# Performance work log

Measured on AMD Instinct MI355X. Metric: run time of the kernel, lower is better.

The kernel has to match this reference:

```python
import jax, jax.numpy as jnp
import numpy as np

NUM_CONN = 8

def _ein_reduce(f):
    # Einstein t-norm fold over last axis: T(a,b) = ab / (2 - (a+b-ab))
    acc = f[..., 0]
    for i in range(1, f.shape[-1]):
        b = f[..., i]
        ab = acc * b
        acc = ab / (2.0 - (acc + b - ab))
    return acc

def _coein_reduce(f):
    # Einstein t-conorm fold over last axis: S(a,b) = (a+b) / (1 + ab)
    acc = f[..., 0]
    for i in range(1, f.shape[-1]):
        b = f[..., i]
        acc = (acc + b) / (1.0 + acc * b)
    return acc

def _ddlg_layer(x, w, idx, is_train):
    # x: [B, in], idx: [out, C] int, w: [out, 4]
    feats = x[:, idx]                      # [B, out, C] gather
    ops = jnp.stack([
        jnp.min(feats, axis=-1),
        jnp.max(feats, axis=-1),
        _ein_reduce(feats),
        _coein_reduce(feats),
    ], axis=-1)                            # [B, out, 4]
    if is_train:
        prob = jax.nn.softmax(w, axis=-1)  # [out, 4]
    else:
        prob = jax.nn.one_hot(jnp.argmax(w, axis=-1), 4, dtype=x.dtype)
    return jnp.einsum('bof,of->bo', ops, prob)

def setup_inputs() -> dict:
    key = jax.random.key(0)
    ks = jax.random.split(key, 6)
    sizes = [4096, 2048, 1024, 2048, 4096]
    x = jax.random.uniform(ks[0], (4096, sizes[0]), dtype=jnp.float32)
    ws = [jax.random.normal(ks[1 + i], (sizes[i + 1], 4), dtype=jnp.float32) for i in range(4)]
    rng = np.random.default_rng(0)
    idxs = []
    for i in range(4):
        # randperm-without-replacement per output neuron
        perm = np.argsort(rng.random((sizes[i + 1], sizes[i])), axis=-1)[:, :NUM_CONN]
        idxs.append(jnp.asarray(perm, dtype=jnp.int32))
    return {
        'x': x,
        'w0': ws[0], 'w1': ws[1], 'w2': ws[2], 'w3': ws[3],
        'idx0': idxs[0], 'idx1': idxs[1], 'idx2': idxs[2], 'idx3': idxs[3],
        'is_train': 1,
    }

def reference(x, w0, w1, w2, w3, idx0, idx1, idx2, idx3, is_train):
    h = _ddlg_layer(x, w0, idx0, is_train)
    h = _ddlg_layer(h, w1, idx1, is_train)
    h = _ddlg_layer(h, w2, idx2, is_train)
    h = _ddlg_layer(h, w3, idx3, is_train)
    return h
```

## Files before the change

### kernel.cpp

```cpp
#include <hip/hip_runtime.h>


typedef _Float16 h2 __attribute__((ext_vector_type(2)));
typedef _Float16 h4 __attribute__((ext_vector_type(4)));

__device__ __forceinline__ float fastrcp(float x) { return __builtin_amdgcn_rcpf(x); }
__device__ __forceinline__ _Float16 hrcp(_Float16 x) {
#if __has_builtin(__builtin_amdgcn_rcph)
    return __builtin_amdgcn_rcph(x);
#else
    return (_Float16)__builtin_amdgcn_rcpf((float)x);
#endif
}
__device__ __forceinline__ h2 splat2(_Float16 s) { h2 v = {s, s}; return v; }
__device__ __forceinline__ unsigned packh2(float a, float b) {
    h2 v = {(_Float16)a, (_Float16)b};
    return __builtin_bit_cast(unsigned, v);
}

__global__ __launch_bounds__(256) void prep_k(const float* __restrict__ w0,
                                              const float* __restrict__ w1,
                                              const float* __restrict__ w2,
                                              const float* __restrict__ w3,
                                              const int* __restrict__ is_train,
                                              h4* __restrict__ probsH) {
    const int g = blockIdx.x * 256 + threadIdx.x;
    const float* w; int o;
    if (g < 2048)      { w = w0; o = g; }
    else if (g < 3072) { w = w1; o = g - 2048; }
    else if (g < 5120) { w = w2; o = g - 3072; }
    else               { w = w3; o = g - 5120; }
    float wv[4];
#pragma unroll
    for (int c = 0; c < 4; ++c) wv[c] = w[(o << 2) + c];
    float p[4];
    if (*is_train) {
        float m = fmaxf(fmaxf(wv[0], wv[1]), fmaxf(wv[2], wv[3]));
        float s = 0.0f;
#pragma unroll
        for (int c = 0; c < 4; ++c) { p[c] = __expf(wv[c] - m); s += p[c]; }
        float inv = fastrcp(s);
#pragma unroll
        for (int c = 0; c < 4; ++c) p[c] *= inv;
    } else {
        int a = 0; float best = wv[0];
#pragma unroll
        for (int c = 1; c < 4; ++c) if (wv[c] > best) { best = wv[c]; a = c; }
#pragma unroll
        for (int c = 0; c < 4; ++c) p[c] = (c == a) ? 1.0f : 0.0f;
    }
    probsH[g] = h4{(_Float16)p[0], (_Float16)p[1], (_Float16)p[2], (_Float16)p[3]};
}

struct Chain { h2 mn, mx, De, Ne, Nc, Dc; };

__device__ __forceinline__ h2 row_at(const unsigned* __restrict__ rows, int i) {
    return __builtin_bit_cast(h2, rows[i]);
}
__device__ __forceinline__ void cinit(Chain& C, h2 v) {
    const h2 one = splat2((_Float16)1.0f), two = splat2((_Float16)2.0f);
    C.mn = v; C.mx = v; C.De = v;
    C.Ne = two - v; C.Nc = one + v; C.Dc = one - v;
}
__device__ __forceinline__ void cstep(Chain& C, h2 v) {
    const h2 two = splat2((_Float16)2.0f);
    C.mn = __builtin_elementwise_min(C.mn, v);
    C.mx = __builtin_elementwise_max(C.mx, v);
    C.De *= v;
    C.Ne *= (two - v);
    C.Nc += C.Nc * v;
    C.Dc -= C.Dc * v;
}
__device__ __forceinline__ h2 finale(const Chain& C, h4 P) {
    h2 s1 = C.Ne + C.De;
    h2 s2 = C.Nc + C.Dc;
    h2 d1 = C.Nc - C.Dc;
    h2 ss = s1 * s2;
    h2 r  = {hrcp(ss[0]), hrcp(ss[1])};
    h2 t1 = (C.De + C.De) * s2;
    h2 t2 = d1 * s1;
    h2 num = splat2(P[2]) * t1 + splat2(P[3]) * t2;
    return splat2(P[0]) * C.mn + splat2(P[1]) * C.mx + num * r;
}

__device__ __forceinline__ h2 gate(const unsigned* __restrict__ rows,
                                   const int4* __restrict__ idx,
                                   const h4* __restrict__ probs, int o) {
    const int4 i0 = idx[o * 2], i1 = idx[o * 2 + 1];
    const h4 P = probs[o];
    h2 A[8];
    A[0] = row_at(rows, i0.x); A[1] = row_at(rows, i0.y);
    A[2] = row_at(rows, i0.z); A[3] = row_at(rows, i0.w);
    A[4] = row_at(rows, i1.x); A[5] = row_at(rows, i1.y);
    A[6] = row_at(rows, i1.z); A[7] = row_at(rows, i1.w);
    Chain C; cinit(C, A[0]);
#pragma unroll
    for (int c = 1; c < 8; ++c) cstep(C, A[c]);
    return finale(C, P);
}

__global__ __launch_bounds__(512, 8) void ddlg_fused(const float* __restrict__ x,
                                                     const h4* __restrict__ probsH,
                                                     const int4* __restrict__ idx0,
                                                     const int4* __restrict__ idx1,
                                                     const int4* __restrict__ idx2,
                                                     const int4* __restrict__ idx3,
                                                     float* __restrict__ out) {
    __shared__ __align__(16) unsigned lds[6144];
    const int t  = threadIdx.x;
    const int b0 = blockIdx.x << 1;

    const unsigned* xl  = lds;
    const unsigned* h0v = lds + 4096;
    const unsigned* h1v = lds;
    const unsigned* h2v = lds + 4096;

#pragma unroll
    for (int c = 0; c < 8; ++c) {
        const int j = (c << 9) + t;
        const float v0 = x[(size_t)(b0 + 0) * 4096 + j];
        const float v1 = x[(size_t)(b0 + 1) * 4096 + j];
        lds[j] = packh2(v0, v1);
    }
    __syncthreads();

#pragma unroll
    for (int k = 0; k < 4; ++k) {
        const int o = (k << 9) + t;
        h2 r = gate(xl, idx0, probsH, o);
        lds[4096 + o] = __builtin_bit_cast(unsigned, r);
    }
    __syncthreads();

#pragma unroll
    for (int k = 0; k < 2; ++k) {
        const int o = (k << 9) + t;
        h2 r = gate(h0v, idx1, probsH + 2048, o);
        lds[o] = __builtin_bit_cast(unsigned, r);
    }
    __syncthreads();

#pragma unroll
    for (int k = 0; k < 4; ++k) {
        const int o = (k << 9) + t;
        h2 r = gate(h1v, idx2, probsH + 3072, o);
        lds[4096 + o] = __builtin_bit_cast(unsigned, r);
    }
    __syncthreads();

#pragma unroll
    for (int k = 0; k < 8; ++k) {
        const int o = (k << 9) + t;
        h2 r = gate(h2v, idx3, probsH + 5120, o);
        out[(size_t)(b0 + 0) * 4096 + o] = (float)r[0];
        out[(size_t)(b0 + 1) * 4096 + o] = (float)r[1];
    }
}

extern "C" void kernel_launch(void* const* d_in, const int* in_sizes, int n_in,
                              void* d_out, int out_size, void* d_ws, size_t ws_size,
                              hipStream_t stream) {
    const float* x        = (const float*)d_in[0];
    const float* w0       = (const float*)d_in[1];
    const float* w1       = (const float*)d_in[2];
    const float* w2       = (const float*)d_in[3];
    const float* w3       = (const float*)d_in[4];
    const int4*  idx0     = (const int4*)d_in[5];
    const int4*  idx1     = (const int4*)d_in[6];
    const int4*  idx2     = (const int4*)d_in[7];
    const int4*  idx3     = (const int4*)d_in[8];
    const int*   is_train = (const int*)d_in[9];
    float*       out      = (float*)d_out;

    h4* probsH = (h4*)d_ws;

    prep_k<<<36, 256, 0, stream>>>(w0, w1, w2, w3, is_train, probsH);
    ddlg_fused<<<2048, 512, 0, stream>>>(x, probsH, idx0, idx1, idx2, idx3, out);
}
```

Baseline: 167.2 us.

## Process four batch rows per block with 8-byte LDS gathers and inline packed-f16 asm

Each block now handles four batch rows instead of two, packing them as two half2 words per LDS slot, so every gathered index loads 8 bytes and the index and probability loads are shared across twice as many rows. The chain arithmetic is written as inline v_pk_* f16 assembly to control instruction selection. Blocks grow to 1024 threads with 48KB of LDS, which halves the grid and may reduce how many blocks fit on a CU. Inline asm also stops the compiler from scheduling or fusing those operations.

```diff
diff --git a/kernel.cpp b/kernel.cpp
--- a/kernel.cpp
+++ b/kernel.cpp
@@ -17,6 +17,38 @@
     h2 v = {(_Float16)a, (_Float16)b};
     return __builtin_bit_cast(unsigned, v);
 }
+
+__device__ __forceinline__ unsigned pk_min(unsigned a, unsigned b) {
+    unsigned d; asm("v_pk_min_f16 %0, %1, %2" : "=v"(d) : "v"(a), "v"(b)); return d;
+}
+__device__ __forceinline__ unsigned pk_max(unsigned a, unsigned b) {
+    unsigned d; asm("v_pk_max_f16 %0, %1, %2" : "=v"(d) : "v"(a), "v"(b)); return d;
+}
+__device__ __forceinline__ unsigned pk_mul(unsigned a, unsigned b) {
+    unsigned d; asm("v_pk_mul_f16 %0, %1, %2" : "=v"(d) : "v"(a), "v"(b)); return d;
+}
+__device__ __forceinline__ unsigned pk_add(unsigned a, unsigned b) {
+    unsigned d; asm("v_pk_add_f16 %0, %1, %2" : "=v"(d) : "v"(a), "v"(b)); return d;
+}
+__device__ __forceinline__ unsigned pk_sub(unsigned a, unsigned b) {
+    unsigned d;
+    asm("v_pk_add_f16 %0, %1, %2 neg_lo:[0,1] neg_hi:[0,1]" : "=v"(d) : "v"(a), "v"(b));
+    return d;
+}
+__device__ __forceinline__ unsigned pk_fma(unsigned a, unsigned b, unsigned c) {
+    unsigned d;
+    asm("v_pk_fma_f16 %0, %1, %2, %3" : "=v"(d) : "v"(a), "v"(b), "v"(c));
+    return d;
+}
+__device__ __forceinline__ unsigned pk_fnma(unsigned a, unsigned b, unsigned c) {
+    unsigned d;
+    asm("v_pk_fma_f16 %0, %1, %2, %3 neg_lo:[1,0,0] neg_hi:[1,0,0]"
+        : "=v"(d) : "v"(a), "v"(b), "v"(c));
+    return d;
+}
+
+#define PK_ONE 0x3C003C00u
+#define PK_TWO 0x40004000u
 
 __global__ __launch_bounds__(256) void prep_k(const float* __restrict__ w0,
                                               const float* __restrict__ w1,
@@ -52,108 +84,114 @@
     probsH[g] = h4{(_Float16)p[0], (_Float16)p[1], (_Float16)p[2], (_Float16)p[3]};
 }
 
-struct Chain { h2 mn, mx, De, Ne, Nc, Dc; };
-
-__device__ __forceinline__ h2 row_at(const unsigned* __restrict__ rows, int i) {
-    return __builtin_bit_cast(h2, rows[i]);
-}
-__device__ __forceinline__ void cinit(Chain& C, h2 v) {
-    const h2 one = splat2((_Float16)1.0f), two = splat2((_Float16)2.0f);
-    C.mn = v; C.mx = v; C.De = v;
-    C.Ne = two - v; C.Nc = one + v; C.Dc = one - v;
-}
-__device__ __forceinline__ void cstep(Chain& C, h2 v) {
-    const h2 two = splat2((_Float16)2.0f);
-    C.mn = __builtin_elementwise_min(C.mn, v);
-    C.mx = __builtin_elementwise_max(C.mx, v);
-    C.De *= v;
-    C.Ne *= (two - v);
-    C.Nc += C.Nc * v;
-    C.Dc -= C.Dc * v;
-}
-__device__ __forceinline__ h2 finale(const Chain& C, h4 P) {
-    h2 s1 = C.Ne + C.De;
-    h2 s2 = C.Nc + C.Dc;
-    h2 d1 = C.Nc - C.Dc;
-    h2 ss = s1 * s2;
-    h2 r  = {hrcp(ss[0]), hrcp(ss[1])};
-    h2 t1 = (C.De + C.De) * s2;
-    h2 t2 = d1 * s1;
-    h2 num = splat2(P[2]) * t1 + splat2(P[3]) * t2;
-    return splat2(P[0]) * C.mn + splat2(P[1]) * C.mx + num * r;
-}
-
-__device__ __forceinline__ h2 gate(const unsigned* __restrict__ rows,
-                                   const int4* __restrict__ idx,
-                                   const h4* __restrict__ probs, int o) {
+struct Chain { unsigned mn0, mn1, mx0, mx1, De0, De1, Ne0, Ne1, Nc0, Nc1, Dc0, Dc1; };
+
+__device__ __forceinline__ void cinit(Chain& C, uint2 v) {
+    C.mn0 = v.x; C.mx0 = v.x; C.De0 = v.x;
+    C.Ne0 = pk_sub(PK_TWO, v.x); C.Nc0 = pk_add(PK_ONE, v.x); C.Dc0 = pk_sub(PK_ONE, v.x);
+    C.mn1 = v.y; C.mx1 = v.y; C.De1 = v.y;
+    C.Ne1 = pk_sub(PK_TWO, v.y); C.Nc1 = pk_add(PK_ONE, v.y); C.Dc1 = pk_sub(PK_ONE, v.y);
+}
+__device__ __forceinline__ void cstep(Chain& C, uint2 v) {
+    C.mn0 = pk_min(C.mn0, v.x);            C.mn1 = pk_min(C.mn1, v.y);
+    C.mx0 = pk_max(C.mx0, v.x);            C.mx1 = pk_max(C.mx1, v.y);
+    C.De0 = pk_mul(C.De0, v.x);            C.De1 = pk_mul(C.De1, v.y);
+    const unsigned w0 = pk_sub(PK_TWO, v.x), w1 = pk_sub(PK_TWO, v.y);
+    C.Ne0 = pk_mul(C.Ne0, w0);             C.Ne1 = pk_mul(C.Ne1, w1);
+    C.Nc0 = pk_fma(C.Nc0, v.x, C.Nc0);     C.Nc1 = pk_fma(C.Nc1, v.y, C.Nc1);
+    C.Dc0 = pk_fnma(C.Dc0, v.x, C.Dc0);    C.Dc1 = pk_fnma(C.Dc1, v.y, C.Dc1);
+}
+
+__device__ __forceinline__ h2 ash2(unsigned u) { return __builtin_bit_cast(h2, u); }
+
+__device__ __forceinline__ uint2 finale(const Chain& C, h4 P) {
+    h2 s10 = ash2(C.Ne0) + ash2(C.De0), s11 = ash2(C.Ne1) + ash2(C.De1);
+    h2 s20 = ash2(C.Nc0) + ash2(C.Dc0), s21 = ash2(C.Nc1) + ash2(C.Dc1);
+    h2 d10 = ash2(C.Nc0) - ash2(C.Dc0), d11 = ash2(C.Nc1) - ash2(C.Dc1);
+    h2 ss0 = s10 * s20,                 ss1 = s11 * s21;
+    h2 r0 = {hrcp(ss0[0]), hrcp(ss0[1])};
+    h2 r1 = {hrcp(ss1[0]), hrcp(ss1[1])};
+    h2 t10 = (ash2(C.De0) + ash2(C.De0)) * s20;
+    h2 t11 = (ash2(C.De1) + ash2(C.De1)) * s21;
+    h2 t20 = d10 * s10, t21 = d11 * s11;
+    const h2 P0 = splat2(P[0]), P1 = splat2(P[1]);
+    const h2 P2 = splat2(P[2]), P3 = splat2(P[3]);
+    h2 num0 = P2 * t10 + P3 * t20;
+    h2 num1 = P2 * t11 + P3 * t21;
+    h2 lo = P0 * ash2(C.mn0) + P1 * ash2(C.mx0) + num0 * r0;
+    h2 hi = P0 * ash2(C.mn1) + P1 * ash2(C.mx1) + num1 * r1;
+    return uint2{__builtin_bit_cast(unsigned, lo), __builtin_bit_cast(unsigned, hi)};
+}
+
+__device__ __forceinline__ uint2 gate(const uint2* __restrict__ rows,
+                                      const int4* __restrict__ idx,
+                                      const h4* __restrict__ probs, int o) {
     const int4 i0 = idx[o * 2], i1 = idx[o * 2 + 1];
     const h4 P = probs[o];
-    h2 A[8];
-    A[0] = row_at(rows, i0.x); A[1] = row_at(rows, i0.y);
-    A[2] = row_at(rows, i0.z); A[3] = row_at(rows, i0.w);
-    A[4] = row_at(rows, i1.x); A[5] = row_at(rows, i1.y);
-    A[6] = row_at(rows, i1.z); A[7] = row_at(rows, i1.w);
+    uint2 A[8];
+    A[0] = rows[i0.x]; A[1] = rows[i0.y]; A[2] = rows[i0.z]; A[3] = rows[i0.w];
+    A[4] = rows[i1.x]; A[5] = rows[i1.y]; A[6] = rows[i1.z]; A[7] = rows[i1.w];
     Chain C; cinit(C, A[0]);
 #pragma unroll
     for (int c = 1; c < 8; ++c) cstep(C, A[c]);
     return finale(C, P);
 }
 
-__global__ __launch_bounds__(512, 8) void ddlg_fused(const float* __restrict__ x,
-                                                     const h4* __restrict__ probsH,
-                                                     const int4* __restrict__ idx0,
-                                                     const int4* __restrict__ idx1,
-                                                     const int4* __restrict__ idx2,
-                                                     const int4* __restrict__ idx3,
-                                                     float* __restrict__ out) {
-    __shared__ __align__(16) unsigned lds[6144];
+__global__ __launch_bounds__(1024, 8) void ddlg_fused(const float* __restrict__ x,
+                                                      const h4* __restrict__ probsH,
+                                                      const int4* __restrict__ idx0,
+                                                      const int4* __restrict__ idx1,
+                                                      const int4* __restrict__ idx2,
+                                                      const int4* __restrict__ idx3,
+                                                      float* __restrict__ out) {
+    __shared__ __align__(16) _Float16 lds[24576];
     const int t  = threadIdx.x;
-    const int b0 = blockIdx.x << 1;
-
-    const unsigned* xl  = lds;
-    const unsigned* h0v = lds + 4096;
-    const unsigned* h1v = lds;
-    const unsigned* h2v = lds + 4096;
-
-#pragma unroll
-    for (int c = 0; c < 8; ++c) {
-        const int j = (c << 9) + t;
+    const int b0 = blockIdx.x << 2;
+
+    const uint2* xl  = (const uint2*)lds;
+    const uint2* h0v = (const uint2*)(lds + 16384);
+    const uint2* h1v = (const uint2*)lds;
+    const uint2* h2v = (const uint2*)(lds + 16384);
+    uint2* const h0w = (uint2*)(lds + 16384);
+    uint2* const h1w = (uint2*)lds;
+
+#pragma unroll
+    for (int c = 0; c < 4; ++c) {
+        const int j = (c << 10) + t;
         const float v0 = x[(size_t)(b0 + 0) * 4096 + j];
         const float v1 = x[(size_t)(b0 + 1) * 4096 + j];
-        lds[j] = packh2(v0, v1);
+        const float v2 = x[(size_t)(b0 + 2) * 4096 + j];
+        const float v3 = x[(size_t)(b0 + 3) * 4096 + j];
+        ((uint2*)lds)[j] = uint2{packh2(v0, v1), packh2(v2, v3)};
+    }
+    __syncthreads();
+
+#pragma unroll
+    for (int k = 0; k < 2; ++k) {
+        const int o = (k << 10) + t;
+        h0w[o] = gate(xl, idx0, probsH, o);
+    }
+    __syncthreads();
+
+    h1w[t] = gate(h0v, idx1, probsH + 2048, t);
+    __syncthreads();
+
+#pragma unroll
+    for (int k = 0; k < 2; ++k) {
+        const int o = (k << 10) + t;
+        h0w[o] = gate(h1v, idx2, probsH + 3072, o);
     }
     __syncthreads();
 
 #pragma unroll
     for (int k = 0; k < 4; ++k) {
-        const int o = (k << 9) + t;
-        h2 r = gate(xl, idx0, probsH, o);
-        lds[4096 + o] = __builtin_bit_cast(unsigned, r);
-    }
-    __syncthreads();
-
-#pragma unroll
-    for (int k = 0; k < 2; ++k) {
-        const int o = (k << 9) + t;
-        h2 r = gate(h0v, idx1, probsH + 2048, o);
-        lds[o] = __builtin_bit_cast(unsigned, r);
-    }
-    __syncthreads();
-
-#pragma unroll
-    for (int k = 0; k < 4; ++k) {
-        const int o = (k << 9) + t;
-        h2 r = gate(h1v, idx2, probsH + 3072, o);
-        lds[4096 + o] = __builtin_bit_cast(unsigned, r);
-    }
-    __syncthreads();
-
-#pragma unroll
-    for (int k = 0; k < 8; ++k) {
-        const int o = (k << 9) + t;
-        h2 r = gate(h2v, idx3, probsH + 5120, o);
-        out[(size_t)(b0 + 0) * 4096 + o] = (float)r[0];
-        out[(size_t)(b0 + 1) * 4096 + o] = (float)r[1];
+        const int o = (k << 10) + t;
+        uint2 r = gate(h2v, idx3, probsH + 5120, o);
+        h2 lo = ash2(r.x), hi = ash2(r.y);
+        out[(size_t)(b0 + 0) * 4096 + o] = (float)lo[0];
+        out[(size_t)(b0 + 1) * 4096 + o] = (float)lo[1];
+        out[(size_t)(b0 + 2) * 4096 + o] = (float)hi[0];
+        out[(size_t)(b0 + 3) * 4096 + o] = (float)hi[1];
     }
 }
 
@@ -175,5 +213,5 @@
     h4* probsH = (h4*)d_ws;
 
     prep_k<<<36, 256, 0, stream>>>(w0, w1, w2, w3, is_train, probsH);
-    ddlg_fused<<<2048, 512, 0, stream>>>(x, probsH, idx0, idx1, idx2, idx3, out);
-}
+    ddlg_fused<<<1024, 1024, 0, stream>>>(x, probsH, idx0, idx1, idx2, idx3, out);
+}
```

New measurement: 160.9 us. 1.04x faster.
